# Kernel tuning notes

Measured on AMD Instinct MI355X. Metric: run time of the kernel, lower is better.

The kernel has to match this reference:

```python
import jax, jax.numpy as jnp
import numpy as np

DIM_EMB = 512
NB_HEADS = 16
NB_LAYERS = 3
BSZ = 256
NB_NODES = 500
NEG_INF = -1e9


def my_mha(q, K, V, nb_heads, mask=None, clip_value=None):
    # q: (bsz, 1, d); K, V: (bsz, n, d); mask: (bsz, n) bool (True = masked)
    bsz, n, d = K.shape
    dh = d // nb_heads
    qh = q.reshape(bsz, nb_heads, dh)            # split emb into heads
    Kh = K.reshape(bsz, n, nb_heads, dh)
    Vh = V.reshape(bsz, n, nb_heads, dh)
    scores = jnp.einsum('bhd,bnhd->bhn', qh, Kh) / jnp.sqrt(jnp.asarray(dh, q.dtype))
    if clip_value is not None:
        scores = clip_value * jnp.tanh(scores)
    if mask is not None:
        scores = jnp.where(mask[:, None, :], jnp.asarray(NEG_INF, scores.dtype), scores)
    w = jax.nn.softmax(scores, axis=-1)          # (bsz, H, n)
    out = jnp.einsum('bhn,bnhd->bhd', w, Vh).reshape(bsz, 1, d)
    attn_weights = w.mean(axis=1)[:, None, :]    # (bsz, 1, n)
    return out, attn_weights


def setup_inputs() -> dict:
    key = jax.random.key(0)
    ks = jax.random.split(key, 5)
    s = 1.0 / np.sqrt(DIM_EMB)
    return {
        'query': jax.random.normal(ks[0], (BSZ, 1, DIM_EMB), jnp.float32),
        'K_att': jax.random.normal(ks[1], (BSZ, NB_NODES, DIM_EMB * NB_LAYERS), jnp.float32),
        'V_att': jax.random.normal(ks[2], (BSZ, NB_NODES, DIM_EMB * NB_LAYERS), jnp.float32),
        'mask': jnp.zeros((BSZ, NB_NODES), jnp.bool_),
        'W0_w': jax.random.normal(ks[3], (DIM_EMB, DIM_EMB), jnp.float32) * s,
        'W0_b': jnp.zeros((DIM_EMB,), jnp.float32),
        'Wqf_w': jax.random.normal(ks[4], (DIM_EMB, DIM_EMB), jnp.float32) * s,
        'Wqf_b': jnp.zeros((DIM_EMB,), jnp.float32),
    }


def reference(query, K_att, V_att, mask, W0_w, W0_b, Wqf_w, Wqf_b):
    d = DIM_EMB
    attn_weights = None
    for l in range(NB_LAYERS):
        K_l = K_att[:, :, l * d:(l + 1) * d]
        V_l = V_att[:, :, l * d:(l + 1) * d]
        if l < NB_LAYERS - 1:
            out, _ = my_mha(query, K_l, V_l, NB_HEADS, mask)
            query = out @ W0_w.T + W0_b
        else:
            q_final = (query @ Wqf_w.T + Wqf_b).reshape(-1, 1, d)
            _, attn_weights = my_mha(q_final, K_l, V_l, 1, mask, clip_value=10.0)
    return attn_weights[:, 0, :]  # (bsz, nb_nodes)
```

## Files before the change

kernel.cpp:

```cpp
#include <hip/hip_runtime.h>
#include <cstdint>
#include <cstddef>

#define BSZ 256
#define NN 500
#define D 512
#define H 16
#define KSTRIDE 1536
#define NEG_INF -1000000000.0f

#define WS_WT0   0
#define WS_WCT   262144
#define WS_BC    524288

__global__ __launch_bounds__(256) void prep(
    const float* __restrict__ W0, const float* __restrict__ Wqf,
    const float* __restrict__ b0, const float* __restrict__ bqf,
    float* __restrict__ Wt0, float* __restrict__ Wct, float* __restrict__ bc)
{
    __shared__ float As[32][33];
    __shared__ float Bs[32][33];

    const int t  = threadIdx.x;
    const int bx = blockIdx.x, by = blockIdx.y;

    if (blockIdx.z == 0) {
        const int tx = t & 31, ty = t >> 5;
        const int c0 = bx * 32, r0 = by * 32;
#pragma unroll
        for (int i = 0; i < 32; i += 8)
            As[ty + i][tx] = W0[(size_t)(r0 + ty + i) * D + c0 + tx];
        __syncthreads();
#pragma unroll
        for (int i = 0; i < 32; i += 8)
            Wt0[(size_t)(c0 + ty + i) * D + r0 + tx] = As[tx][ty + i];
        return;
    }

    const int j0 = by * 32;
    const int d0 = bx * 32;
    const int lr  = t >> 3;
    const int lc4 = (t & 7) * 4;
    const int ty2 = (t >> 4) * 2;
    const int tx2 = (t & 15) * 2;

    float c00 = 0.f, c01 = 0.f, c10 = 0.f, c11 = 0.f;

    for (int k0 = 0; k0 < D; k0 += 32) {
        const float4 av = *reinterpret_cast<const float4*>(
            Wqf + (size_t)(j0 + lr) * D + k0 + lc4);
        const float4 bv = *reinterpret_cast<const float4*>(
            W0 + (size_t)(k0 + lr) * D + d0 + lc4);
        As[lr][lc4] = av.x; As[lr][lc4 + 1] = av.y;
        As[lr][lc4 + 2] = av.z; As[lr][lc4 + 3] = av.w;
        Bs[lr][lc4] = bv.x; Bs[lr][lc4 + 1] = bv.y;
        Bs[lr][lc4 + 2] = bv.z; Bs[lr][lc4 + 3] = bv.w;
        __syncthreads();
#pragma unroll 8
        for (int kk = 0; kk < 32; ++kk) {
            const float a0 = As[ty2][kk], a1 = As[ty2 + 1][kk];
            const float v0 = Bs[kk][tx2], v1 = Bs[kk][tx2 + 1];
            c00 += a0 * v0; c01 += a0 * v1;
            c10 += a1 * v0; c11 += a1 * v1;
        }
        __syncthreads();
    }

    As[tx2][ty2]         = c00;
    As[tx2 + 1][ty2]     = c01;
    As[tx2][ty2 + 1]     = c10;
    As[tx2 + 1][ty2 + 1] = c11;
    __syncthreads();
#pragma unroll
    for (int i = 0; i < 4; ++i)
        Wct[(size_t)(d0 + lr) * D + j0 + lc4 + i] = As[lr][lc4 + i];

    if (bx == 0 && t < 32) {
        const int j = j0 + t;
        float s = 0.f;
        for (int k = 0; k < D; ++k)
            s += Wqf[(size_t)j * D + k] * b0[k];
        bc[j] = s + bqf[j];
    }
}

__device__ __forceinline__ float4 ld4(const float* p) {
    return *reinterpret_cast<const float4*>(p);
}

__device__ __forceinline__ float head_score(const float4 qa, const float4 qb,
                                            const float4 k0, const float4 k1)
{
    float s = qa.x * k0.x + qa.y * k0.y + qa.z * k0.z + qa.w * k0.w
            + qb.x * k1.x + qb.y * k1.y + qb.z * k1.z + qb.w * k1.w;
    s += __shfl_xor(s, 1);
    s += __shfl_xor(s, 2);
    return s * 0.17677669529663687f;
}

__device__ __forceinline__ void online_upd(float& m, float& l, float4& a0, float4& a1,
                                           const float sc, const float4 v0, const float4 v1)
{
    const float mn   = fmaxf(m, sc);
    const float corr = __expf(m - mn);
    const float e    = __expf(sc - mn);
    l = l * corr + e;
    a0.x = a0.x * corr + e * v0.x;
    a0.y = a0.y * corr + e * v0.y;
    a0.z = a0.z * corr + e * v0.z;
    a0.w = a0.w * corr + e * v0.w;
    a1.x = a1.x * corr + e * v1.x;
    a1.y = a1.y * corr + e * v1.y;
    a1.z = a1.z * corr + e * v1.z;
    a1.w = a1.w * corr + e * v1.w;
    m = mn;
}

__device__ __forceinline__ void stream_attn(
    const float4 qa, const float4 qb,
    const float* __restrict__ Kb, const float* __restrict__ Vb,
    const unsigned char* __restrict__ mask_lds,
    const int g, const int r,
    float* __restrict__ part_acc, float* __restrict__ part_m,
    float* __restrict__ part_l)
{
    float mA = -3.4e38f, lA = 0.f;
    float4 aA0 = {0.f,0.f,0.f,0.f}, aA1 = {0.f,0.f,0.f,0.f};
    float mB = -3.4e38f, lB = 0.f;
    float4 aB0 = {0.f,0.f,0.f,0.f}, aB1 = {0.f,0.f,0.f,0.f};

    for (int n = g; n < NN; n += 32) {
        const int n2 = n + 16;
        const float* krA = Kb + (size_t)n * KSTRIDE + r * 8;
        const float* vrA = Vb + (size_t)n * KSTRIDE + r * 8;
        const float4 kA0 = ld4(krA), kA1 = ld4(krA + 4);
        const float4 vA0 = ld4(vrA), vA1 = ld4(vrA + 4);

        if (n2 < NN) {
            const float* krB = Kb + (size_t)n2 * KSTRIDE + r * 8;
            const float* vrB = Vb + (size_t)n2 * KSTRIDE + r * 8;
            const float4 kB0 = ld4(krB), kB1 = ld4(krB + 4);
            const float4 vB0 = ld4(vrB), vB1 = ld4(vrB + 4);

            float scA = head_score(qa, qb, kA0, kA1);
            if (mask_lds[n]) scA = NEG_INF;
            online_upd(mA, lA, aA0, aA1, scA, vA0, vA1);

            float scB = head_score(qa, qb, kB0, kB1);
            if (mask_lds[n2]) scB = NEG_INF;
            online_upd(mB, lB, aB0, aB1, scB, vB0, vB1);
        } else {
            float scA = head_score(qa, qb, kA0, kA1);
            if (mask_lds[n]) scA = NEG_INF;
            online_upd(mA, lA, aA0, aA1, scA, vA0, vA1);
        }
    }

    const float mn = fmaxf(mA, mB);
    const float wA = __expf(mA - mn), wB = __expf(mB - mn);
    const float lm = lA * wA + lB * wB;
    float4 o0, o1;
    o0.x = aA0.x * wA + aB0.x * wB;  o0.y = aA0.y * wA + aB0.y * wB;
    o0.z = aA0.z * wA + aB0.z * wB;  o0.w = aA0.w * wA + aB0.w * wB;
    o1.x = aA1.x * wA + aB1.x * wB;  o1.y = aA1.y * wA + aB1.y * wB;
    o1.z = aA1.z * wA + aB1.z * wB;  o1.w = aA1.w * wA + aB1.w * wB;

    *reinterpret_cast<float4*>(part_acc + g * D + r * 8)     = o0;
    *reinterpret_cast<float4*>(part_acc + g * D + r * 8 + 4) = o1;
    if ((r & 3) == 0) {
        part_m[g * H + (r >> 2)] = mn;
        part_l[g * H + (r >> 2)] = lm;
    }
}

__global__ __launch_bounds__(1024) void fused_all(
    const float* __restrict__ query,
    const float* __restrict__ Katt,
    const float* __restrict__ Vatt,
    const unsigned char* __restrict__ mask,
    const float* __restrict__ Wt0, const float* __restrict__ b0,
    const float* __restrict__ Wct, const float* __restrict__ bc,
    float* __restrict__ out)
{
    __shared__ __align__(16) float part_acc[16 * D];
    __shared__ float part_m[16 * H];
    __shared__ float part_l[16 * H];
    __shared__ __align__(16) float out_lds[D];
    __shared__ __align__(16) float q_lds[D];
    __shared__ float gemv_part[2 * D];
    __shared__ unsigned char mask_lds[512];
    __shared__ float s_lds[NN];
    __shared__ float red[16];
    __shared__ float bm, bs;

    const int b = blockIdx.x;
    const int t = threadIdx.x;
    const int r = t & 63;
    const int g = t >> 6;

    if (t < 512) mask_lds[t] = (t < NN) ? mask[(size_t)b * NN + t] : 0;

    const float* Kbase = Katt + (size_t)b * NN * KSTRIDE;
    const float* Vbase = Vatt + (size_t)b * NN * KSTRIDE;

    float4 qa = ld4(query + (size_t)b * D + r * 8);
    float4 qb = ld4(query + (size_t)b * D + r * 8 + 4);
    __syncthreads();

#pragma unroll 1
    for (int layer = 0; layer < 2; ++layer) {
        const int loff = layer * 512;
        stream_attn(qa, qb, Kbase + loff, Vbase + loff, mask_lds, g, r,
                    part_acc, part_m, part_l);
        __syncthreads();

        if (t < D) {
            const int hd = t >> 5;
            float ms = -3.4e38f;
#pragma unroll
            for (int g2 = 0; g2 < 16; ++g2)
                ms = fmaxf(ms, part_m[g2 * H + hd]);
            float ls = 0.f, o = 0.f;
#pragma unroll
            for (int g2 = 0; g2 < 16; ++g2) {
                const float w = __expf(part_m[g2 * H + hd] - ms);
                ls += part_l[g2 * H + hd] * w;
                o  += part_acc[g2 * D + t] * w;
            }
            out_lds[t] = o / ls;
        }
        __syncthreads();

        {
            const float* Wt   = layer ? Wct : Wt0;
            const float* bias = layer ? bc  : b0;
            const int j = t & 511;
            const int half = t >> 9;
            const float* Wp = Wt + (size_t)half * 256 * D + j;
            const float* a  = out_lds + half * 256;
            float acc = 0.f;
#pragma unroll 4
            for (int k = 0; k < 256; ++k)
                acc += a[k] * Wp[(size_t)k * D];
            gemv_part[half * D + j] = acc;
            __syncthreads();
            if (t < D) q_lds[t] = gemv_part[t] + gemv_part[D + t] + bias[t];
            __syncthreads();
        }

        qa = ld4(q_lds + r * 8);
        qb = ld4(q_lds + r * 8 + 4);
    }

    {
        const int wv   = t >> 6;
        const int l    = t & 63;
        const int half = l >> 5;
        const int l32  = l & 31;

        const float* qpp = q_lds + l32 * 16;
        const float4 f0 = ld4(qpp);
        const float4 f1 = ld4(qpp + 4);
        const float4 f2 = ld4(qpp + 8);
        const float4 f3 = ld4(qpp + 12);

        const float* Kb2 = Kbase + 1024;

        for (int n = wv * 2 + half; n < NN; n += 32) {
            const float* kr = Kb2 + (size_t)n * KSTRIDE + l32 * 16;
            const float4 k0 = ld4(kr);
            const float4 k1 = ld4(kr + 4);
            const float4 k2 = ld4(kr + 8);
            const float4 k3 = ld4(kr + 12);
            float s = f0.x * k0.x + f0.y * k0.y + f0.z * k0.z + f0.w * k0.w
                    + f1.x * k1.x + f1.y * k1.y + f1.z * k1.z + f1.w * k1.w
                    + f2.x * k2.x + f2.y * k2.y + f2.z * k2.z + f2.w * k2.w
                    + f3.x * k3.x + f3.y * k3.y + f3.z * k3.z + f3.w * k3.w;
#pragma unroll
            for (int o = 1; o < 32; o <<= 1) s += __shfl_xor(s, o);
            if (l32 == 0) {
                float sc = 10.0f * tanhf(s * 0.044194173824159216f);
                if (mask_lds[n]) sc = NEG_INF;
                s_lds[n] = sc;
            }
        }
        __syncthreads();

        const float v = (t < NN) ? s_lds[t] : -3.4e38f;
        float m = v;
#pragma unroll
        for (int o = 1; o < 64; o <<= 1) m = fmaxf(m, __shfl_xor(m, o));
        if (l == 0) red[wv] = m;
        __syncthreads();
        if (t == 0) {
            float mm = red[0];
#pragma unroll
            for (int i = 1; i < 16; ++i) mm = fmaxf(mm, red[i]);
            bm = mm;
        }
        __syncthreads();
        const float e = (t < NN) ? __expf(v - bm) : 0.f;
        float ssum = e;
#pragma unroll
        for (int o = 1; o < 64; o <<= 1) ssum += __shfl_xor(ssum, o);
        if (l == 0) red[wv] = ssum;
        __syncthreads();
        if (t == 0) {
            float s2 = 0.f;
#pragma unroll
            for (int i = 0; i < 16; ++i) s2 += red[i];
            bs = 1.0f / s2;
        }
        __syncthreads();
        if (t < NN) out[(size_t)b * NN + t] = e * bs;
    }
}

extern "C" void kernel_launch(void* const* d_in, const int* in_sizes, int n_in,
                              void* d_out, int out_size, void* d_ws, size_t ws_size,
                              hipStream_t stream) {
    const float* query = (const float*)d_in[0];
    const float* Katt  = (const float*)d_in[1];
    const float* Vatt  = (const float*)d_in[2];
    const unsigned char* mask = (const unsigned char*)d_in[3];
    const float* W0w = (const float*)d_in[4];
    const float* W0b = (const float*)d_in[5];
    const float* Wfw = (const float*)d_in[6];
    const float* Wfb = (const float*)d_in[7];

    float* out = (float*)d_out;
    float* ws  = (float*)d_ws;
    float* Wt0 = ws + WS_WT0;
    float* Wct = ws + WS_WCT;
    float* bc  = ws + WS_BC;

    prep<<<dim3(16, 16, 2), 256, 0, stream>>>(W0w, Wfw, W0b, Wfb, Wt0, Wct, bc);
    fused_all<<<BSZ, 1024, 0, stream>>>(query, Katt, Vatt, mask,
                                        Wt0, W0b, Wct, bc, out);
}
```

Baseline: 309.0 us.

## Drop online softmax max tracking, unfold composed weight, use nontemporal loads

The attention streaming loop drops the running-max online softmax and accumulates exp(score) directly. This removes the per-node correction exps and the cross-group max merge, but it can overflow if scores are large or if every node is masked. The prep kernel no longer precomputes the composed Wqf·W0 matrix and bias. It only transposes both weights, and the fused kernel now runs two GEMVs per batch for the final query. K/V and output accesses switch to nontemporal loads and stores, and the node loop is fully unrolled with fixed trip counts.

```diff
diff --git a/kernel.cpp b/kernel.cpp
--- a/kernel.cpp
+++ b/kernel.cpp
@@ -10,82 +10,34 @@
 #define NEG_INF -1000000000.0f
 
 #define WS_WT0   0
-#define WS_WCT   262144
-#define WS_BC    524288
-
-__global__ __launch_bounds__(256) void prep(
+#define WS_WTF   262144
+
+typedef float f32x4 __attribute__((ext_vector_type(4)));
+
+__global__ __launch_bounds__(256) void prep_transpose(
     const float* __restrict__ W0, const float* __restrict__ Wqf,
-    const float* __restrict__ b0, const float* __restrict__ bqf,
-    float* __restrict__ Wt0, float* __restrict__ Wct, float* __restrict__ bc)
-{
-    __shared__ float As[32][33];
-    __shared__ float Bs[32][33];
-
-    const int t  = threadIdx.x;
-    const int bx = blockIdx.x, by = blockIdx.y;
-
-    if (blockIdx.z == 0) {
-        const int tx = t & 31, ty = t >> 5;
-        const int c0 = bx * 32, r0 = by * 32;
-#pragma unroll
-        for (int i = 0; i < 32; i += 8)
-            As[ty + i][tx] = W0[(size_t)(r0 + ty + i) * D + c0 + tx];
-        __syncthreads();
-#pragma unroll
-        for (int i = 0; i < 32; i += 8)
-            Wt0[(size_t)(c0 + ty + i) * D + r0 + tx] = As[tx][ty + i];
-        return;
-    }
-
-    const int j0 = by * 32;
-    const int d0 = bx * 32;
-    const int lr  = t >> 3;
-    const int lc4 = (t & 7) * 4;
-    const int ty2 = (t >> 4) * 2;
-    const int tx2 = (t & 15) * 2;
-
-    float c00 = 0.f, c01 = 0.f, c10 = 0.f, c11 = 0.f;
-
-    for (int k0 = 0; k0 < D; k0 += 32) {
-        const float4 av = *reinterpret_cast<const float4*>(
-            Wqf + (size_t)(j0 + lr) * D + k0 + lc4);
-        const float4 bv = *reinterpret_cast<const float4*>(
-            W0 + (size_t)(k0 + lr) * D + d0 + lc4);
-        As[lr][lc4] = av.x; As[lr][lc4 + 1] = av.y;
-        As[lr][lc4 + 2] = av.z; As[lr][lc4 + 3] = av.w;
-        Bs[lr][lc4] = bv.x; Bs[lr][lc4 + 1] = bv.y;
-        Bs[lr][lc4 + 2] = bv.z; Bs[lr][lc4 + 3] = bv.w;
-        __syncthreads();
-#pragma unroll 8
-        for (int kk = 0; kk < 32; ++kk) {
-            const float a0 = As[ty2][kk], a1 = As[ty2 + 1][kk];
-            const float v0 = Bs[kk][tx2], v1 = Bs[kk][tx2 + 1];
-            c00 += a0 * v0; c01 += a0 * v1;
-            c10 += a1 * v0; c11 += a1 * v1;
-        }
-        __syncthreads();
-    }
-
-    As[tx2][ty2]         = c00;
-    As[tx2 + 1][ty2]     = c01;
-    As[tx2][ty2 + 1]     = c10;
-    As[tx2 + 1][ty2 + 1] = c11;
-    __syncthreads();
-#pragma unroll
-    for (int i = 0; i < 4; ++i)
-        Wct[(size_t)(d0 + lr) * D + j0 + lc4 + i] = As[lr][lc4 + i];
-
-    if (bx == 0 && t < 32) {
-        const int j = j0 + t;
-        float s = 0.f;
-        for (int k = 0; k < D; ++k)
-            s += Wqf[(size_t)j * D + k] * b0[k];
-        bc[j] = s + bqf[j];
-    }
+    float* __restrict__ Wt0, float* __restrict__ Wtf)
+{
+    __shared__ float tile[32][33];
+    const float* in = blockIdx.z ? Wqf : W0;
+    float* out      = blockIdx.z ? Wtf : Wt0;
+    const int bx = blockIdx.x * 32, by = blockIdx.y * 32;
+    const int tx = threadIdx.x & 31, ty = threadIdx.x >> 5;
+#pragma unroll
+    for (int i = 0; i < 32; i += 8)
+        tile[ty + i][tx] = in[(size_t)(by + ty + i) * D + bx + tx];
+    __syncthreads();
+#pragma unroll
+    for (int i = 0; i < 32; i += 8)
+        out[(size_t)(bx + ty + i) * D + by + tx] = tile[tx][ty + i];
 }
 
 __device__ __forceinline__ float4 ld4(const float* p) {
     return *reinterpret_cast<const float4*>(p);
+}
+__device__ __forceinline__ float4 ld4nt(const float* p) {
+    f32x4 v = __builtin_nontemporal_load(reinterpret_cast<const f32x4*>(p));
+    return float4{v.x, v.y, v.z, v.w};
 }
 
 __device__ __forceinline__ float head_score(const float4 qa, const float4 qb,
@@ -98,22 +50,29 @@
     return s * 0.17677669529663687f;
 }
 
-__device__ __forceinline__ void online_upd(float& m, float& l, float4& a0, float4& a1,
-                                           const float sc, const float4 v0, const float4 v1)
-{
-    const float mn   = fmaxf(m, sc);
-    const float corr = __expf(m - mn);
-    const float e    = __expf(sc - mn);
-    l = l * corr + e;
-    a0.x = a0.x * corr + e * v0.x;
-    a0.y = a0.y * corr + e * v0.y;
-    a0.z = a0.z * corr + e * v0.z;
-    a0.w = a0.w * corr + e * v0.w;
-    a1.x = a1.x * corr + e * v1.x;
-    a1.y = a1.y * corr + e * v1.y;
-    a1.z = a1.z * corr + e * v1.z;
-    a1.w = a1.w * corr + e * v1.w;
-    m = mn;
+__device__ __forceinline__ void upd(float& l, float4& a0, float4& a1,
+                                    const float sc, const float4 v0, const float4 v1)
+{
+    const float e = __expf(sc);
+    l += e;
+    a0.x += e * v0.x; a0.y += e * v0.y; a0.z += e * v0.z; a0.w += e * v0.w;
+    a1.x += e * v1.x; a1.y += e * v1.y; a1.z += e * v1.z; a1.w += e * v1.w;
+}
+
+__device__ __forceinline__ void do_node(
+    const float4 qa, const float4 qb,
+    const float* __restrict__ Kb, const float* __restrict__ Vb,
+    const unsigned char* __restrict__ mask_lds,
+    const int n, const int r,
+    float& l, float4& a0, float4& a1)
+{
+    const float* kr = Kb + (size_t)n * KSTRIDE + r * 8;
+    const float* vr = Vb + (size_t)n * KSTRIDE + r * 8;
+    const float4 k0 = ld4nt(kr), k1 = ld4nt(kr + 4);
+    const float4 v0 = ld4nt(vr), v1 = ld4nt(vr + 4);
+    float sc = head_score(qa, qb, k0, k1);
+    if (mask_lds[n]) sc = NEG_INF;
+    upd(l, a0, a1, sc, v0, v1);
 }
 
 __device__ __forceinline__ void stream_attn(
@@ -121,56 +80,50 @@
     const float* __restrict__ Kb, const float* __restrict__ Vb,
     const unsigned char* __restrict__ mask_lds,
     const int g, const int r,
-    float* __restrict__ part_acc, float* __restrict__ part_m,
-    float* __restrict__ part_l)
-{
-    float mA = -3.4e38f, lA = 0.f;
+    float* __restrict__ part_acc, float* __restrict__ part_l)
+{
+    float lA = 0.f, lB = 0.f;
     float4 aA0 = {0.f,0.f,0.f,0.f}, aA1 = {0.f,0.f,0.f,0.f};
-    float mB = -3.4e38f, lB = 0.f;
     float4 aB0 = {0.f,0.f,0.f,0.f}, aB1 = {0.f,0.f,0.f,0.f};
 
-    for (int n = g; n < NN; n += 32) {
-        const int n2 = n + 16;
-        const float* krA = Kb + (size_t)n * KSTRIDE + r * 8;
-        const float* vrA = Vb + (size_t)n * KSTRIDE + r * 8;
-        const float4 kA0 = ld4(krA), kA1 = ld4(krA + 4);
-        const float4 vA0 = ld4(vrA), vA1 = ld4(vrA + 4);
-
-        if (n2 < NN) {
-            const float* krB = Kb + (size_t)n2 * KSTRIDE + r * 8;
-            const float* vrB = Vb + (size_t)n2 * KSTRIDE + r * 8;
-            const float4 kB0 = ld4(krB), kB1 = ld4(krB + 4);
-            const float4 vB0 = ld4(vrB), vB1 = ld4(vrB + 4);
-
-            float scA = head_score(qa, qb, kA0, kA1);
-            if (mask_lds[n]) scA = NEG_INF;
-            online_upd(mA, lA, aA0, aA1, scA, vA0, vA1);
-
-            float scB = head_score(qa, qb, kB0, kB1);
-            if (mask_lds[n2]) scB = NEG_INF;
-            online_upd(mB, lB, aB0, aB1, scB, vB0, vB1);
-        } else {
-            float scA = head_score(qa, qb, kA0, kA1);
-            if (mask_lds[n]) scA = NEG_INF;
-            online_upd(mA, lA, aA0, aA1, scA, vA0, vA1);
-        }
+    for (int i = 0; i < 15; ++i) {
+        const int n = g + i * 32;
+        do_node(qa, qb, Kb, Vb, mask_lds, n,      r, lA, aA0, aA1);
+        do_node(qa, qb, Kb, Vb, mask_lds, n + 16, r, lB, aB0, aB1);
     }
-
-    const float mn = fmaxf(mA, mB);
-    const float wA = __expf(mA - mn), wB = __expf(mB - mn);
-    const float lm = lA * wA + lB * wB;
+    do_node(qa, qb, Kb, Vb, mask_lds, g + 480, r, lA, aA0, aA1);
+    if (g < 4)
+        do_node(qa, qb, Kb, Vb, mask_lds, g + 496, r, lB, aB0, aB1);
+
     float4 o0, o1;
-    o0.x = aA0.x * wA + aB0.x * wB;  o0.y = aA0.y * wA + aB0.y * wB;
-    o0.z = aA0.z * wA + aB0.z * wB;  o0.w = aA0.w * wA + aB0.w * wB;
-    o1.x = aA1.x * wA + aB1.x * wB;  o1.y = aA1.y * wA + aB1.y * wB;
-    o1.z = aA1.z * wA + aB1.z * wB;  o1.w = aA1.w * wA + aB1.w * wB;
+    o0.x = aA0.x + aB0.x;  o0.y = aA0.y + aB0.y;
+    o0.z = aA0.z + aB0.z;  o0.w = aA0.w + aB0.w;
+    o1.x = aA1.x + aB1.x;  o1.y = aA1.y + aB1.y;
+    o1.z = aA1.z + aB1.z;  o1.w = aA1.w + aB1.w;
 
     *reinterpret_cast<float4*>(part_acc + g * D + r * 8)     = o0;
     *reinterpret_cast<float4*>(part_acc + g * D + r * 8 + 4) = o1;
-    if ((r & 3) == 0) {
-        part_m[g * H + (r >> 2)] = mn;
-        part_l[g * H + (r >> 2)] = lm;
-    }
+    if ((r & 3) == 0)
+        part_l[g * H + (r >> 2)] = lA + lB;
+}
+
+__device__ __forceinline__ void gemv(
+    const float* __restrict__ a_lds, const float* __restrict__ Wt,
+    const float* __restrict__ bias, float* __restrict__ dst_lds,
+    float* __restrict__ gemv_part, const int t)
+{
+    const int j = t & 511;
+    const int half = t >> 9;
+    const float* Wp = Wt + (size_t)half * 256 * D + j;
+    const float* a  = a_lds + half * 256;
+    float acc = 0.f;
+#pragma unroll 4
+    for (int k = 0; k < 256; ++k)
+        acc += a[k] * Wp[(size_t)k * D];
+    gemv_part[half * D + j] = acc;
+    __syncthreads();
+    if (t < D) dst_lds[t] = gemv_part[t] + gemv_part[D + t] + bias[t];
+    __syncthreads();
 }
 
 __global__ __launch_bounds__(1024) void fused_all(
@@ -179,13 +132,13 @@
     const float* __restrict__ Vatt,
     const unsigned char* __restrict__ mask,
     const float* __restrict__ Wt0, const float* __restrict__ b0,
-    const float* __restrict__ Wct, const float* __restrict__ bc,
+    const float* __restrict__ Wtf, const float* __restrict__ bf,
     float* __restrict__ out)
 {
     __shared__ __align__(16) float part_acc[16 * D];
-    __shared__ float part_m[16 * H];
     __shared__ float part_l[16 * H];
     __shared__ __align__(16) float out_lds[D];
+    __shared__ __align__(16) float mid_lds[D];
     __shared__ __align__(16) float q_lds[D];
     __shared__ float gemv_part[2 * D];
     __shared__ unsigned char mask_lds[512];
@@ -209,43 +162,27 @@
 
 #pragma unroll 1
     for (int layer = 0; layer < 2; ++layer) {
-        const int loff = layer * 512;
-        stream_attn(qa, qb, Kbase + loff, Vbase + loff, mask_lds, g, r,
-                    part_acc, part_m, part_l);
+        stream_attn(qa, qb, Kbase + layer * 512, Vbase + layer * 512,
+                    mask_lds, g, r, part_acc, part_l);
         __syncthreads();
 
         if (t < D) {
             const int hd = t >> 5;
-            float ms = -3.4e38f;
-#pragma unroll
-            for (int g2 = 0; g2 < 16; ++g2)
-                ms = fmaxf(ms, part_m[g2 * H + hd]);
             float ls = 0.f, o = 0.f;
 #pragma unroll
             for (int g2 = 0; g2 < 16; ++g2) {
-                const float w = __expf(part_m[g2 * H + hd] - ms);
-                ls += part_l[g2 * H + hd] * w;
-                o  += part_acc[g2 * D + t] * w;
+                ls += part_l[g2 * H + hd];
+                o  += part_acc[g2 * D + t];
             }
             out_lds[t] = o / ls;
         }
         __syncthreads();
 
-        {
-            const float* Wt   = layer ? Wct : Wt0;
-            const float* bias = layer ? bc  : b0;
-            const int j = t & 511;
-            const int half = t >> 9;
-            const float* Wp = Wt + (size_t)half * 256 * D + j;
-            const float* a  = out_lds + half * 256;
-            float acc = 0.f;
-#pragma unroll 4
-            for (int k = 0; k < 256; ++k)
-                acc += a[k] * Wp[(size_t)k * D];
-            gemv_part[half * D + j] = acc;
-            __syncthreads();
-            if (t < D) q_lds[t] = gemv_part[t] + gemv_part[D + t] + bias[t];
-            __syncthreads();
+        if (layer == 0) {
+            gemv(out_lds, Wt0, b0, q_lds, gemv_part, t);
+        } else {
+            gemv(out_lds, Wt0, b0, mid_lds, gemv_part, t);
+            gemv(mid_lds, Wtf, bf, q_lds, gemv_part, t);
         }
 
         qa = ld4(q_lds + r * 8);
@@ -268,10 +205,10 @@
 
         for (int n = wv * 2 + half; n < NN; n += 32) {
             const float* kr = Kb2 + (size_t)n * KSTRIDE + l32 * 16;
-            const float4 k0 = ld4(kr);
-            const float4 k1 = ld4(kr + 4);
-            const float4 k2 = ld4(kr + 8);
-            const float4 k3 = ld4(kr + 12);
+            const float4 k0 = ld4nt(kr);
+            const float4 k1 = ld4nt(kr + 4);
+            const float4 k2 = ld4nt(kr + 8);
+            const float4 k3 = ld4nt(kr + 12);
             float s = f0.x * k0.x + f0.y * k0.y + f0.z * k0.z + f0.w * k0.w
                     + f1.x * k1.x + f1.y * k1.y + f1.z * k1.z + f1.w * k1.w
                     + f2.x * k2.x + f2.y * k2.y + f2.z * k2.z + f2.w * k2.w
@@ -312,7 +249,8 @@
             bs = 1.0f / s2;
         }
         __syncthreads();
-        if (t < NN) out[(size_t)b * NN + t] = e * bs;
+        if (t < NN)
+            __builtin_nontemporal_store(e * bs, out + (size_t)b * NN + t);
     }
 }
 
@@ -331,10 +269,9 @@
     float* out = (float*)d_out;
     float* ws  = (float*)d_ws;
     float* Wt0 = ws + WS_WT0;
-    float* Wct = ws + WS_WCT;
-    float* bc  = ws + WS_BC;
-
-    prep<<<dim3(16, 16, 2), 256, 0, stream>>>(W0w, Wfw, W0b, Wfb, Wt0, Wct, bc);
+    float* Wtf = ws + WS_WTF;
+
+    prep_transpose<<<dim3(16, 16, 2), 256, 0, stream>>>(W0w, Wfw, Wt0, Wtf);
     fused_all<<<BSZ, 1024, 0, stream>>>(query, Katt, Vatt, mask,
-                                        Wt0, W0b, Wct, bc, out);
-}
+                                        Wt0, W0b, Wtf, Wfb, out);
+}
```

Result: faster. 294.3 us (-4.8%).
